# Kernel tuning notes

Measured on AMD Instinct MI355X. Metric: run time of the kernel, lower is better.

Reference implementation:

```python
import jax, jax.numpy as jnp
import numpy as np
from jax import lax

# Config matching init_kwargs
POOL_K, POOL_S, POOL_P = 3, 2, 1
UNF_K, UNF_S, UNF_P = 5, 4, 1


def setup_inputs() -> dict:
    key = jax.random.key(0)
    x = jax.random.normal(key, (32, 3, 512, 512), dtype=jnp.float32)
    return {"x": x}


def reference(x):
    # 1) MaxPool2d(k=3, s=2, p=1); torch pads with -inf for max pooling
    neg_inf = jnp.array(-jnp.inf, dtype=x.dtype)
    pooled = lax.reduce_window(
        x, neg_inf, lax.max,
        window_dimensions=(1, 1, POOL_K, POOL_K),
        window_strides=(1, 1, POOL_S, POOL_S),
        padding=[(0, 0), (0, 0), (POOL_P, POOL_P), (POOL_P, POOL_P)],
    )
    # 2) per-channel global context -> SiLU gate, shape (N, C, 1, 1)
    gate = jax.nn.silu(pooled.mean(axis=(2, 3), keepdims=True))
    # 3) Unfold(k=5, s=4, p=1) followed by mean over the K*K patch pixels.
    #    Zero padding + mean over all K*K entries == windowed sum / K^2
    #    (avg pool with count_include_pad). Fused: never materialize im2col.
    zero = jnp.array(0.0, dtype=x.dtype)
    win_sum = lax.reduce_window(
        x, zero, lax.add,
        window_dimensions=(1, 1, UNF_K, UNF_K),
        window_strides=(1, 1, UNF_S, UNF_S),
        padding=[(0, 0), (0, 0), (UNF_P, UNF_P), (UNF_P, UNF_P)],
    )
    # 4) gate each patch (per-channel) and average -> (N, C, H_out, W_out)
    out = (win_sum / (UNF_K * UNF_K)) * gate
    return out
```

## Files before the change

kernel.cpp:

```cpp
#include <hip/hip_runtime.h>
#include <math.h>

#define H 512
#define W 512
#define PH 256
#define PW 256
#define OH 128
#define OW 128
#define NPLANES 96
#define TILES_PER_PLANE 16
#define WS_PARTIALS 0
#define WS_WSUM 2048

__device__ __forceinline__ float4 fmax4(float4 a, float4 b) {
    return make_float4(fmaxf(a.x, b.x), fmaxf(a.y, b.y),
                       fmaxf(a.z, b.z), fmaxf(a.w, b.w));
}
__device__ __forceinline__ float4 fadd4(float4 a, float4 b) {
    return make_float4(a.x + b.x, a.y + b.y, a.z + b.z, a.w + b.w);
}
__device__ __forceinline__ float hsum4(float4 a) {
    return a.x + a.y + a.z + a.w;
}

__global__ __launch_bounds__(256, 4) void fused_kernel(
    const float* __restrict__ x, float* __restrict__ ws) {
    const int bx = blockIdx.x;
    const int plane = bx / TILES_PER_PLANE;
    const int sub = bx % TILES_PER_PLANE;
    const float* __restrict__ p = x + (size_t)plane * (H * W);
    const int wid = threadIdx.x >> 6;
    const int lane = threadIdx.x & 63;
    const int t = sub * 4 + wid;
    const int col = lane << 3;

    float4 a[9], b[9];
    #pragma unroll
    for (int j = 0; j < 9; ++j) {
        int r = 8 * t - 1 + j;
        if (r < 0) r = 0;
        const float* rp = p + r * W + col;
        a[j] = *(const float4*)(rp);
        b[j] = *(const float4*)(rp + 4);
    }

    float acc = 0.f;
    #pragma unroll
    for (int k = 0; k < 4; ++k) {
        float4 va = fmax4(fmax4(a[2 * k], a[2 * k + 1]), a[2 * k + 2]);
        float4 vb = fmax4(fmax4(b[2 * k], b[2 * k + 1]), b[2 * k + 2]);
        float vL = __shfl_up(vb.w, 1, 64);
        if (lane == 0) vL = va.x;
        acc += fmaxf(fmaxf(vL, va.x), va.y);
        acc += fmaxf(fmaxf(va.y, va.z), va.w);
        acc += fmaxf(fmaxf(va.w, vb.x), vb.y);
        acc += fmaxf(fmaxf(vb.y, vb.z), vb.w);
    }
    #pragma unroll
    for (int off = 32; off > 0; off >>= 1)
        acc += __shfl_down(acc, off, 64);
    __shared__ float smem[4];
    if (lane == 0) smem[wid] = acc;

    float4 z = make_float4(0.f, 0.f, 0.f, 0.f);
    float4 a0 = (t == 0) ? z : a[0];
    float4 b0 = (t == 0) ? z : b[0];
    float4 sa0 = fadd4(fadd4(fadd4(a0, a[1]), fadd4(a[2], a[3])), a[4]);
    float4 sb0 = fadd4(fadd4(fadd4(b0, b[1]), fadd4(b[2], b[3])), b[4]);
    float4 sa1 = fadd4(fadd4(fadd4(a[4], a[5]), fadd4(a[6], a[7])), a[8]);
    float4 sb1 = fadd4(fadd4(fadd4(b[4], b[5]), fadd4(b[6], b[7])), b[8]);

    float* wrow = ws + WS_WSUM + (size_t)plane * (OH * OW);
    {
        float sL = __shfl_up(sb0.w, 1, 64);
        if (lane == 0) sL = 0.f;
        float o0 = sL + hsum4(sa0);
        float o1 = sa0.w + hsum4(sb0);
        *(float2*)&wrow[(2 * t) * OW + 2 * lane] = make_float2(o0, o1);
    }
    {
        float sL = __shfl_up(sb1.w, 1, 64);
        if (lane == 0) sL = 0.f;
        float o0 = sL + hsum4(sa1);
        float o1 = sa1.w + hsum4(sb1);
        *(float2*)&wrow[(2 * t + 1) * OW + 2 * lane] = make_float2(o0, o1);
    }

    __syncthreads();
    if (threadIdx.x == 0) {
        ws[WS_PARTIALS + plane * TILES_PER_PLANE + sub] =
            smem[0] + smem[1] + smem[2] + smem[3];
    }
}

__global__ __launch_bounds__(256) void scale_kernel(
    const float* __restrict__ ws, float* __restrict__ out) {
    const int bx = blockIdx.x;
    const int plane = bx >> 2;
    const int quarter = bx & 3;

    float s = 0.f;
    #pragma unroll
    for (int i = 0; i < TILES_PER_PLANE; ++i)
        s += ws[WS_PARTIALS + plane * TILES_PER_PLANE + i];
    s *= (1.0f / (float)(PH * PW));
    const float gate = s / (1.0f + expf(-s));
    const float scale = gate * (1.0f / 25.0f);

    const float4* src = (const float4*)(ws + WS_WSUM + (size_t)plane * (OH * OW));
    float4* dst = (float4*)(out + (size_t)plane * (OH * OW));
    const int base = quarter * 1024 + threadIdx.x;
    #pragma unroll
    for (int i = 0; i < 4; ++i) {
        const int idx = base + i * 256;
        float4 v = src[idx];
        dst[idx] = make_float4(v.x * scale, v.y * scale,
                               v.z * scale, v.w * scale);
    }
}

extern "C" void kernel_launch(void* const* d_in, const int* in_sizes, int n_in,
                              void* d_out, int out_size, void* d_ws, size_t ws_size,
                              hipStream_t stream) {
    const float* x = (const float*)d_in[0];
    float* out = (float*)d_out;
    float* ws = (float*)d_ws;

    fused_kernel<<<NPLANES * TILES_PER_PLANE, 256, 0, stream>>>(x, ws);
    scale_kernel<<<NPLANES * 4, 256, 0, stream>>>(ws, out);
}
```

Before: 26.17 us.

## Fuse pooling and gating into one cooperative kernel with grid sync

Replaces the two-kernel flow with a single cooperative kernel of 384 blocks. Each block handles four row tiles per wave, keeps the window sums in registers, publishes its max-pool partial, then waits on a grid-wide barrier before scaling and writing the output directly. This removes the workspace round trip for the window sums and the second launch. It adds the cost of a grid sync and lowers occupancy through higher register use. The old two-kernel path stays as a fallback if the cooperative launch fails.

```diff
diff --git a/kernel.cpp b/kernel.cpp
--- a/kernel.cpp
+++ b/kernel.cpp
@@ -1,5 +1,8 @@
 #include <hip/hip_runtime.h>
+#include <hip/hip_cooperative_groups.h>
 #include <math.h>
+
+namespace cg = cooperative_groups;
 
 #define H 512
 #define W 512
@@ -8,9 +11,6 @@
 #define OH 128
 #define OW 128
 #define NPLANES 96
-#define TILES_PER_PLANE 16
-#define WS_PARTIALS 0
-#define WS_WSUM 2048
 
 __device__ __forceinline__ float4 fmax4(float4 a, float4 b) {
     return make_float4(fmaxf(a.x, b.x), fmaxf(a.y, b.y),
@@ -23,11 +23,104 @@
     return a.x + a.y + a.z + a.w;
 }
 
+#define C_BPP 4
+#define C_NBLOCKS (NPLANES * C_BPP)
+
+__global__ __launch_bounds__(256, 2) void fused_all(
+    const float* __restrict__ x, float* __restrict__ ws,
+    float* __restrict__ out) {
+    const int n = blockIdx.x;
+    const int bx = (n & 7) * (C_NBLOCKS / 8) + (n >> 3);
+    const int plane = bx / C_BPP;
+    const int sub = bx % C_BPP;
+    const float* __restrict__ p = x + (size_t)plane * (H * W);
+    const int wid = threadIdx.x >> 6;
+    const int lane = threadIdx.x & 63;
+    const int col = lane << 3;
+
+    float acc = 0.f;
+    float2 oo[4][2];
+
+    #pragma unroll
+    for (int u = 0; u < 4; ++u) {
+        const int t = sub * 16 + wid * 4 + u;
+        float4 a[9], b[9];
+        #pragma unroll
+        for (int j = 0; j < 9; ++j) {
+            int r = 8 * t - 1 + j;
+            if (r < 0) r = 0;
+            const float* rp = p + r * W + col;
+            a[j] = *(const float4*)(rp);
+            b[j] = *(const float4*)(rp + 4);
+        }
+
+        #pragma unroll
+        for (int k = 0; k < 4; ++k) {
+            float4 va = fmax4(fmax4(a[2 * k], a[2 * k + 1]), a[2 * k + 2]);
+            float4 vb = fmax4(fmax4(b[2 * k], b[2 * k + 1]), b[2 * k + 2]);
+            float vL = __shfl_up(vb.w, 1, 64);
+            if (lane == 0) vL = va.x;
+            acc += fmaxf(fmaxf(vL, va.x), va.y);
+            acc += fmaxf(fmaxf(va.y, va.z), va.w);
+            acc += fmaxf(fmaxf(va.w, vb.x), vb.y);
+            acc += fmaxf(fmaxf(vb.y, vb.z), vb.w);
+        }
+
+        float4 z = make_float4(0.f, 0.f, 0.f, 0.f);
+        float4 a0 = (t == 0) ? z : a[0];
+        float4 b0 = (t == 0) ? z : b[0];
+        float4 sa0 = fadd4(fadd4(fadd4(a0, a[1]), fadd4(a[2], a[3])), a[4]);
+        float4 sb0 = fadd4(fadd4(fadd4(b0, b[1]), fadd4(b[2], b[3])), b[4]);
+        float4 sa1 = fadd4(fadd4(fadd4(a[4], a[5]), fadd4(a[6], a[7])), a[8]);
+        float4 sb1 = fadd4(fadd4(fadd4(b[4], b[5]), fadd4(b[6], b[7])), b[8]);
+
+        float sL0 = __shfl_up(sb0.w, 1, 64);
+        float sL1 = __shfl_up(sb1.w, 1, 64);
+        if (lane == 0) { sL0 = 0.f; sL1 = 0.f; }
+        oo[u][0] = make_float2(sL0 + hsum4(sa0), sa0.w + hsum4(sb0));
+        oo[u][1] = make_float2(sL1 + hsum4(sa1), sa1.w + hsum4(sb1));
+    }
+
+    #pragma unroll
+    for (int off = 32; off > 0; off >>= 1)
+        acc += __shfl_down(acc, off, 64);
+    __shared__ float smem[4];
+    if (lane == 0) smem[wid] = acc;
+    __syncthreads();
+    if (threadIdx.x == 0)
+        ws[plane * C_BPP + sub] = smem[0] + smem[1] + smem[2] + smem[3];
+
+    cg::this_grid().sync();
+
+    float s = ws[plane * C_BPP + (lane & 3)];
+    s += __shfl_xor(s, 1, 64);
+    s += __shfl_xor(s, 2, 64);
+    s *= (1.0f / (float)(PH * PW));
+    const float gate = s / (1.0f + expf(-s));
+    const float scale = gate * (1.0f / 25.0f);
+
+    float* oplane = out + (size_t)plane * (OH * OW);
+    #pragma unroll
+    for (int u = 0; u < 4; ++u) {
+        const int t = sub * 16 + wid * 4 + u;
+        #pragma unroll
+        for (int r = 0; r < 2; ++r) {
+            float2 v = oo[u][r];
+            *(float2*)&oplane[(size_t)(2 * t + r) * OW + 2 * lane] =
+                make_float2(v.x * scale, v.y * scale);
+        }
+    }
+}
+
+#define F_TPP 16
+#define WS_PARTIALS 0
+#define WS_WSUM 2048
+
 __global__ __launch_bounds__(256, 4) void fused_kernel(
     const float* __restrict__ x, float* __restrict__ ws) {
     const int bx = blockIdx.x;
-    const int plane = bx / TILES_PER_PLANE;
-    const int sub = bx % TILES_PER_PLANE;
+    const int plane = bx / F_TPP;
+    const int sub = bx % F_TPP;
     const float* __restrict__ p = x + (size_t)plane * (H * W);
     const int wid = threadIdx.x >> 6;
     const int lane = threadIdx.x & 63;
@@ -74,23 +167,20 @@
     {
         float sL = __shfl_up(sb0.w, 1, 64);
         if (lane == 0) sL = 0.f;
-        float o0 = sL + hsum4(sa0);
-        float o1 = sa0.w + hsum4(sb0);
-        *(float2*)&wrow[(2 * t) * OW + 2 * lane] = make_float2(o0, o1);
+        *(float2*)&wrow[(2 * t) * OW + 2 * lane] =
+            make_float2(sL + hsum4(sa0), sa0.w + hsum4(sb0));
     }
     {
         float sL = __shfl_up(sb1.w, 1, 64);
         if (lane == 0) sL = 0.f;
-        float o0 = sL + hsum4(sa1);
-        float o1 = sa1.w + hsum4(sb1);
-        *(float2*)&wrow[(2 * t + 1) * OW + 2 * lane] = make_float2(o0, o1);
+        *(float2*)&wrow[(2 * t + 1) * OW + 2 * lane] =
+            make_float2(sL + hsum4(sa1), sa1.w + hsum4(sb1));
     }
 
     __syncthreads();
-    if (threadIdx.x == 0) {
-        ws[WS_PARTIALS + plane * TILES_PER_PLANE + sub] =
+    if (threadIdx.x == 0)
+        ws[WS_PARTIALS + plane * F_TPP + sub] =
             smem[0] + smem[1] + smem[2] + smem[3];
-    }
 }
 
 __global__ __launch_bounds__(256) void scale_kernel(
@@ -101,8 +191,8 @@
 
     float s = 0.f;
     #pragma unroll
-    for (int i = 0; i < TILES_PER_PLANE; ++i)
-        s += ws[WS_PARTIALS + plane * TILES_PER_PLANE + i];
+    for (int i = 0; i < F_TPP; ++i)
+        s += ws[WS_PARTIALS + plane * F_TPP + i];
     s *= (1.0f / (float)(PH * PW));
     const float gate = s / (1.0f + expf(-s));
     const float scale = gate * (1.0f / 25.0f);
@@ -126,6 +216,12 @@
     float* out = (float*)d_out;
     float* ws = (float*)d_ws;
 
-    fused_kernel<<<NPLANES * TILES_PER_PLANE, 256, 0, stream>>>(x, ws);
-    scale_kernel<<<NPLANES * 4, 256, 0, stream>>>(ws, out);
-}
+    void* args[] = {(void*)&x, (void*)&ws, (void*)&out};
+    hipError_t err = hipLaunchCooperativeKernel(
+        (const void*)fused_all, dim3(C_NBLOCKS), dim3(256), args, 0, stream);
+    if (err != hipSuccess) {
+        (void)hipGetLastError();
+        fused_kernel<<<NPLANES * F_TPP, 256, 0, stream>>>(x, ws);
+        scale_kernel<<<NPLANES * 4, 256, 0, stream>>>(ws, out);
+    }
+}
```

Measured after the change: 86.82 us. 3.32x slower.

## Split row loads into two phases, raise occupancy and swizzle block order

Applied to the files above, without the earlier changes.

The fused pooling kernel no longer keeps all nine input row pairs live at once. It loads five rows, emits the first output row and max contributions, then reuses those registers for the next four rows. This cuts register pressure so launch bounds can target 8 blocks per SIMD instead of 4. It also remaps block indices with an XCD-style swizzle (n&7 stride) so neighbouring blocks land on different dies. The risk is that the second batch of loads now waits on the first phase's compute, which reduces memory-level parallelism per wave.

```diff
diff --git a/kernel.cpp b/kernel.cpp
--- a/kernel.cpp
+++ b/kernel.cpp
@@ -8,8 +8,10 @@
 #define OH 128
 #define OW 128
 #define NPLANES 96
-#define TILES_PER_PLANE 16
-#define WS_PARTIALS 0
+#define TPP 16
+#define NBLOCKS (NPLANES * TPP)
+
+#define WS_PART 0
 #define WS_WSUM 2048
 
 __device__ __forceinline__ float4 fmax4(float4 a, float4 b) {
@@ -23,74 +25,96 @@
     return a.x + a.y + a.z + a.w;
 }
 
-__global__ __launch_bounds__(256, 4) void fused_kernel(
+__device__ __forceinline__ void hmax_acc(
+    float4 a0, float4 b0, float4 a1, float4 b1, float4 a2, float4 b2,
+    int lane, float& acc) {
+    float4 va = fmax4(fmax4(a0, a1), a2);
+    float4 vb = fmax4(fmax4(b0, b1), b2);
+    float vL = __shfl_up(vb.w, 1, 64);
+    if (lane == 0) vL = va.x;
+    acc += fmaxf(fmaxf(vL, va.x), va.y);
+    acc += fmaxf(fmaxf(va.y, va.z), va.w);
+    acc += fmaxf(fmaxf(va.w, vb.x), vb.y);
+    acc += fmaxf(fmaxf(vb.y, vb.z), vb.w);
+}
+
+__device__ __forceinline__ void emit_row(
+    float4 SA, float4 SB, int lane, float* __restrict__ wrow) {
+    float sL = __shfl_up(SB.w, 1, 64);
+    if (lane == 0) sL = 0.f;
+    *(float2*)&wrow[2 * lane] =
+        make_float2(sL + hsum4(SA), SA.w + hsum4(SB));
+}
+
+__global__ __launch_bounds__(256, 8) void fused_kernel(
     const float* __restrict__ x, float* __restrict__ ws) {
-    const int bx = blockIdx.x;
-    const int plane = bx / TILES_PER_PLANE;
-    const int sub = bx % TILES_PER_PLANE;
-    const float* __restrict__ p = x + (size_t)plane * (H * W);
+    const int n = blockIdx.x;
+    const int bx = (n & 7) * (NBLOCKS / 8) + (n >> 3);
+    const int plane = bx / TPP;
+    const int sub = bx % TPP;
     const int wid = threadIdx.x >> 6;
     const int lane = threadIdx.x & 63;
     const int t = sub * 4 + wid;
-    const int col = lane << 3;
+    const float* __restrict__ base = x + (size_t)plane * (H * W) + (lane << 3);
+    float* __restrict__ wrow = ws + WS_WSUM + (size_t)plane * (OH * OW);
 
-    float4 a[9], b[9];
-    #pragma unroll
-    for (int j = 0; j < 9; ++j) {
-        int r = 8 * t - 1 + j;
-        if (r < 0) r = 0;
-        const float* rp = p + r * W + col;
-        a[j] = *(const float4*)(rp);
-        b[j] = *(const float4*)(rp + 4);
+#define LDROW(va, vb, r)                                            \
+    {                                                               \
+        const float* q = base + (size_t)(r) * W;                    \
+        va = *(const float4*)(q);                                   \
+        vb = *(const float4*)(q + 4);                               \
     }
 
+    float4 A0, B0, A1, B1, A2, B2, A3, B3, A4, B4;
     float acc = 0.f;
-    #pragma unroll
-    for (int k = 0; k < 4; ++k) {
-        float4 va = fmax4(fmax4(a[2 * k], a[2 * k + 1]), a[2 * k + 2]);
-        float4 vb = fmax4(fmax4(b[2 * k], b[2 * k + 1]), b[2 * k + 2]);
-        float vL = __shfl_up(vb.w, 1, 64);
-        if (lane == 0) vL = va.x;
-        acc += fmaxf(fmaxf(vL, va.x), va.y);
-        acc += fmaxf(fmaxf(va.y, va.z), va.w);
-        acc += fmaxf(fmaxf(va.w, vb.x), vb.y);
-        acc += fmaxf(fmaxf(vb.y, vb.z), vb.w);
+
+    {
+        int r0 = 8 * t - 1;
+        if (r0 < 0) r0 = 0;
+        LDROW(A0, B0, r0);
     }
+    LDROW(A1, B1, 8 * t);
+    LDROW(A2, B2, 8 * t + 1);
+    LDROW(A3, B3, 8 * t + 2);
+    LDROW(A4, B4, 8 * t + 3);
+
+    hmax_acc(A0, B0, A1, B1, A2, B2, lane, acc);
+    hmax_acc(A2, B2, A3, B3, A4, B4, lane, acc);
+
+    if (t == 0) {
+        A0 = make_float4(0.f, 0.f, 0.f, 0.f);
+        B0 = make_float4(0.f, 0.f, 0.f, 0.f);
+    }
+    {
+        float4 SA = fadd4(fadd4(fadd4(A0, A1), fadd4(A2, A3)), A4);
+        float4 SB = fadd4(fadd4(fadd4(B0, B1), fadd4(B2, B3)), B4);
+        emit_row(SA, SB, lane, wrow + (size_t)(2 * t) * OW);
+    }
+
+    LDROW(A0, B0, 8 * t + 4);
+    LDROW(A1, B1, 8 * t + 5);
+    LDROW(A2, B2, 8 * t + 6);
+    LDROW(A3, B3, 8 * t + 7);
+
+    hmax_acc(A4, B4, A0, B0, A1, B1, lane, acc);
+    hmax_acc(A1, B1, A2, B2, A3, B3, lane, acc);
+
+    {
+        float4 SA = fadd4(fadd4(fadd4(A4, A0), fadd4(A1, A2)), A3);
+        float4 SB = fadd4(fadd4(fadd4(B4, B0), fadd4(B1, B2)), B3);
+        emit_row(SA, SB, lane, wrow + (size_t)(2 * t + 1) * OW);
+    }
+#undef LDROW
+
     #pragma unroll
     for (int off = 32; off > 0; off >>= 1)
         acc += __shfl_down(acc, off, 64);
     __shared__ float smem[4];
     if (lane == 0) smem[wid] = acc;
-
-    float4 z = make_float4(0.f, 0.f, 0.f, 0.f);
-    float4 a0 = (t == 0) ? z : a[0];
-    float4 b0 = (t == 0) ? z : b[0];
-    float4 sa0 = fadd4(fadd4(fadd4(a0, a[1]), fadd4(a[2], a[3])), a[4]);
-    float4 sb0 = fadd4(fadd4(fadd4(b0, b[1]), fadd4(b[2], b[3])), b[4]);
-    float4 sa1 = fadd4(fadd4(fadd4(a[4], a[5]), fadd4(a[6], a[7])), a[8]);
-    float4 sb1 = fadd4(fadd4(fadd4(b[4], b[5]), fadd4(b[6], b[7])), b[8]);
-
-    float* wrow = ws + WS_WSUM + (size_t)plane * (OH * OW);
-    {
-        float sL = __shfl_up(sb0.w, 1, 64);
-        if (lane == 0) sL = 0.f;
-        float o0 = sL + hsum4(sa0);
-        float o1 = sa0.w + hsum4(sb0);
-        *(float2*)&wrow[(2 * t) * OW + 2 * lane] = make_float2(o0, o1);
-    }
-    {
-        float sL = __shfl_up(sb1.w, 1, 64);
-        if (lane == 0) sL = 0.f;
-        float o0 = sL + hsum4(sa1);
-        float o1 = sa1.w + hsum4(sb1);
-        *(float2*)&wrow[(2 * t + 1) * OW + 2 * lane] = make_float2(o0, o1);
-    }
-
     __syncthreads();
-    if (threadIdx.x == 0) {
-        ws[WS_PARTIALS + plane * TILES_PER_PLANE + sub] =
+    if (threadIdx.x == 0)
+        ws[WS_PART + plane * TPP + sub] =
             smem[0] + smem[1] + smem[2] + smem[3];
-    }
 }
 
 __global__ __launch_bounds__(256) void scale_kernel(
@@ -101,8 +125,8 @@
 
     float s = 0.f;
     #pragma unroll
-    for (int i = 0; i < TILES_PER_PLANE; ++i)
-        s += ws[WS_PARTIALS + plane * TILES_PER_PLANE + i];
+    for (int i = 0; i < TPP; ++i)
+        s += ws[WS_PART + plane * TPP + i];
     s *= (1.0f / (float)(PH * PW));
     const float gate = s / (1.0f + expf(-s));
     const float scale = gate * (1.0f / 25.0f);
@@ -126,6 +150,6 @@
     float* out = (float*)d_out;
     float* ws = (float*)d_ws;
 
-    fused_kernel<<<NPLANES * TILES_PER_PLANE, 256, 0, stream>>>(x, ws);
+    fused_kernel<<<NBLOCKS, 256, 0, stream>>>(x, ws);
     scale_kernel<<<NPLANES * 4, 256, 0, stream>>>(ws, out);
 }
```

After: 28.13 us. 7.5% more time.
